# Performance work log

Measured on AMD Instinct MI355X. Metric: run time of the kernel, lower is better.

## Reference

```python
import jax, jax.numpy as jnp
import numpy as np

B = 65536
D = 512            # resnet18 fc.in_features
NUM_CLASSES = 512  # size of batch_centers
LEVELS = [2048, 1024, 512]


def setup_inputs() -> dict:
    key = jax.random.key(0)
    ks = jax.random.split(key, 8)
    x = jax.random.normal(ks[0], (B, D), dtype=jnp.float32)
    labels = jax.random.randint(ks[1], (B,), 0, NUM_CLASSES, dtype=jnp.int64)
    W0 = jax.random.normal(ks[2], (LEVELS[0], D), dtype=jnp.float32) * 0.02
    b0 = jnp.zeros((LEVELS[0],), dtype=jnp.float32)
    W1 = jax.random.normal(ks[3], (LEVELS[1], LEVELS[0]), dtype=jnp.float32) * 0.02
    b1 = jnp.zeros((LEVELS[1],), dtype=jnp.float32)
    W2 = jax.random.normal(ks[4], (LEVELS[2], LEVELS[1]), dtype=jnp.float32) * 0.02
    b2 = jnp.zeros((LEVELS[2],), dtype=jnp.float32)
    lambda_values = jnp.array([1e-3, 1.0, 1.0, 1.0], dtype=jnp.float32)
    return {"x": x, "W0": W0, "b0": b0, "W1": W1, "b1": b1,
            "W2": W2, "b2": b2, "lambda_values": lambda_values,
            "labels": labels}


def _cross_entropy(logits, labels):
    # mean over batch of -log p(label) (torch CrossEntropyLoss default)
    logp = jax.nn.log_softmax(logits, axis=-1)
    nll = -jnp.take_along_axis(logp, labels[:, None], axis=-1)[:, 0]
    return jnp.mean(nll)


def reference(x, W0, b0, W1, b1, W2, b2, lambda_values, labels):
    # --- per-class scatter-mean centers (vectorized segment reduce) ---
    sums = jax.ops.segment_sum(x, labels, num_segments=NUM_CLASSES)
    counts = jax.ops.segment_sum(jnp.ones((x.shape[0],), x.dtype), labels,
                                 num_segments=NUM_CLASSES)
    centers = jnp.where(counts[:, None] > 0,
                        sums / jnp.maximum(counts, 1.0)[:, None],
                        0.0)  # classes absent from batch keep zero centers
    # --- gather-diff center loss: sum_i ||x_i - c_{y_i}||^2 ---
    diff = x - centers[labels]
    center_loss = jnp.sum(diff * diff)
    # --- cascaded classification heads, CE at each level ---
    h = x
    losses = []
    for W, b in ((W0, b0), (W1, b1), (W2, b2)):
        h = h @ W.T + b
        losses.append(_cross_entropy(h, labels))
    classification_losses = jnp.stack(losses)
    return lambda_values[0] * center_loss + jnp.dot(lambda_values[1:],
                                                    classification_losses)
```

## Files before the change

### kernel.cpp

```cpp
#include <hip/hip_runtime.h>
#include <cstdint>
#include <cstddef>

using f32x4  = __attribute__((ext_vector_type(4))) float;
using i32x4v = __attribute__((ext_vector_type(4))) int;
using i32x8v = __attribute__((ext_vector_type(8))) int;

__device__ __forceinline__ unsigned char f2fp8(float f) {
  return (unsigned char)(__builtin_amdgcn_cvt_pk_fp8_f32(f, f, 0, false) & 0xff);
}

__device__ __forceinline__ float fp8b0(unsigned int w) {
  return __builtin_amdgcn_cvt_f32_fp8(w, 0);
}
__device__ __forceinline__ float fp8b1(unsigned int w) {
  return __builtin_amdgcn_cvt_f32_fp8(w, 1);
}
__device__ __forceinline__ float fp8b2(unsigned int w) {
  return __builtin_amdgcn_cvt_f32_fp8(w, 2);
}
__device__ __forceinline__ float fp8b3(unsigned int w) {
  return __builtin_amdgcn_cvt_f32_fp8(w, 3);
}

__device__ __forceinline__ float waveRed(float v) {
#pragma unroll
  for (int m = 32; m >= 1; m >>= 1) v += __shfl_xor(v, m, 64);
  return v;
}

__device__ __forceinline__ void gload16(const void* g, void* l) {
  __builtin_amdgcn_global_load_lds(
      (__attribute__((address_space(1))) uint32_t*)(uintptr_t)g,
      (__attribute__((address_space(3))) uint32_t*)(uint32_t*)l,
      16, 0, 0);
}

__global__ __launch_bounds__(256) void prep_w(
    const float4* __restrict__ W1, const float4* __restrict__ W2,
    const float4* __restrict__ W0f4, const float* __restrict__ W0,
    const float* __restrict__ b0,
    uint32_t* __restrict__ W1_8, uint32_t* __restrict__ W2_8,
    uint32_t* __restrict__ W0_8, unsigned char* __restrict__ W0t8,
    float* __restrict__ zr, int zwords, float* __restrict__ biascat) {
  __shared__ unsigned char t8[64][65];
  const int b = blockIdx.x;
  const int tid = threadIdx.x;
  if (b < 1024) {
    for (int i = b * 256 + tid; i < 524288; i += 1024 * 256) {
      float4 v = W1[i];
      int p = __builtin_amdgcn_cvt_pk_fp8_f32(v.x, v.y, 0, false);
      p = __builtin_amdgcn_cvt_pk_fp8_f32(v.z, v.w, p, true);
      W1_8[i] = (uint32_t)p;
    }
  } else if (b < 1280) {
    for (int i = (b - 1024) * 256 + tid; i < 131072; i += 256 * 256) {
      float4 v = W2[i];
      int p = __builtin_amdgcn_cvt_pk_fp8_f32(v.x, v.y, 0, false);
      p = __builtin_amdgcn_cvt_pk_fp8_f32(v.z, v.w, p, true);
      W2_8[i] = (uint32_t)p;
    }
  } else if (b < 1536) {
    for (int i = (b - 1280) * 256 + tid; i < 262144; i += 256 * 256) {
      float4 v = W0f4[i];
      int p = __builtin_amdgcn_cvt_pk_fp8_f32(v.x, v.y, 0, false);
      p = __builtin_amdgcn_cvt_pk_fp8_f32(v.z, v.w, p, true);
      W0_8[i] = (uint32_t)p;
    }
  } else if (b < 1792) {
    const int t = b - 1536;
    const int r0 = (t >> 3) * 64, c0 = (t & 7) * 64;
#pragma unroll
    for (int p = 0; p < 16; ++p) {
      const int row = p * 4 + (tid >> 6), col = tid & 63;
      t8[row][col] = f2fp8(W0[(size_t)(r0 + row) * 512 + c0 + col]);
    }
    __syncthreads();
#pragma unroll
    for (int p = 0; p < 16; ++p) {
      const int oc = p * 4 + (tid >> 6), orr = tid & 63;
      W0t8[(size_t)(c0 + oc) * 2048 + r0 + orr] = t8[orr][oc];
    }
  } else {
    const int zb = (zwords + 255) >> 8;
    if (b < 1792 + zb) {
      const int i = (b - 1792) * 256 + tid;
      if (i < zwords) zr[i] = 0.f;
    } else {
      const int i = (b - 1792 - zb) * 256 + tid;
      if (i < 2048) biascat[i] = b0[i];
    }
  }
}

__global__ __launch_bounds__(256) void count_k(const int* __restrict__ lab,
                                               int* __restrict__ counts, int n) {
  __shared__ int h[512];
  for (int i = threadIdx.x; i < 512; i += 256) h[i] = 0;
  __syncthreads();
  for (int i = blockIdx.x * 256 + threadIdx.x; i < n; i += gridDim.x * 256)
    atomicAdd(&h[lab[i]], 1);
  __syncthreads();
  for (int i = threadIdx.x; i < 512; i += 256) {
    int v = h[i];
    if (v) atomicAdd(&counts[i], v);
  }
}

__global__ void prefix_k(const int* __restrict__ counts, int* __restrict__ offsets,
                         int* __restrict__ cursor, int nc) {
  const int lane = threadIdx.x;
  int base = 0;
  for (int c0 = 0; c0 < nc; c0 += 64) {
    int v = counts[c0 + lane];
    int x = v;
#pragma unroll
    for (int d = 1; d < 64; d <<= 1) {
      int y = __shfl_up(x, d, 64);
      if (lane >= d) x += y;
    }
    int excl = base + x - v;
    offsets[c0 + lane] = excl;
    cursor[c0 + lane] = excl;
    base += __shfl(x, 63, 64);
  }
}

__global__ void scatter_k(const int* __restrict__ lab, int* __restrict__ cursor,
                          int* __restrict__ buckets, int n) {
  for (int i = blockIdx.x * 256 + threadIdx.x; i < n; i += gridDim.x * 256) {
    int pos = atomicAdd(&cursor[lab[i]], 1);
    buckets[pos] = i;
  }
}

__global__ __launch_bounds__(256) void csum_k(const float* __restrict__ x,
    const int* __restrict__ buckets, const int* __restrict__ offsets,
    const int* __restrict__ counts, float* __restrict__ centers4,
    float* __restrict__ scal) {
  const int c = blockIdx.x >> 2, q = blockIdx.x & 3;
  const int cnt = counts[c];
  const int t = threadIdx.x;
  float sx = 0.f, sy = 0.f, ssq = 0.f;
  if (cnt) {
    const int beg = offsets[c];
    const int lo = beg + (cnt * q) / 4, hi = beg + (cnt * (q + 1)) / 4;
    for (int i = lo; i < hi; ++i) {
      const int row = buckets[i];
      const float2 v = ((const float2*)(x + (size_t)row * 512))[t];
      sx += v.x;
      sy += v.y;
      ssq += v.x * v.x + v.y * v.y;
    }
  }
  float2* dst = (float2*)(centers4 + (size_t)((c << 2) + q) * 512);
  dst[t] = make_float2(sx, sy);
  ssq = waveRed(ssq);
  __shared__ float red[4];
  if ((t & 63) == 0) red[t >> 6] = ssq;
  __syncthreads();
  if (t == 0) {
    const float s = red[0] + red[1] + red[2] + red[3];
    if (s != 0.f) atomicAdd(&scal[0], s);
  }
}

__global__ __launch_bounds__(256) void cnorm_k(const float* __restrict__ centers4,
    float* __restrict__ centers, const int* __restrict__ counts,
    float* __restrict__ out) {
  const int c = blockIdx.x;
  const int t = threadIdx.x;
  const float2* p = (const float2*)(centers4 + (size_t)(c << 2) * 512);
  float2 s = p[t];
  float2 s1 = p[t + 256], s2 = p[t + 512], s3 = p[t + 768];
  s.x += s1.x + s2.x + s3.x;
  s.y += s1.y + s2.y + s3.y;
  ((float2*)(centers + (size_t)c * 512))[t] = s;
  const int cnt = counts[c];
  if (cnt == 0) return;
  float ssq = s.x * s.x + s.y * s.y;
  ssq = waveRed(ssq);
  __shared__ float red[4];
  if ((t & 63) == 0) red[t >> 6] = ssq;
  __syncthreads();
  if (t == 0)
    atomicAdd(out, (red[0] + red[1] + red[2] + red[3]) / (float)cnt);
}

__global__ __launch_bounds__(256) void matvec_k(const float* __restrict__ W,
    const float* __restrict__ vin, const float* __restrict__ badd,
    float* __restrict__ vout, int K) {
  int row = blockIdx.x;
  float s = 0.f;
  for (int k = threadIdx.x; k < K; k += 256) s += W[(size_t)row * K + k] * vin[k];
  s = waveRed(s);
  __shared__ float red[4];
  if ((threadIdx.x & 63) == 0) red[threadIdx.x >> 6] = s;
  __syncthreads();
  if (threadIdx.x == 0) vout[row] = red[0] + red[1] + red[2] + red[3] + badd[row];
}

__global__ void pk_k(const float* __restrict__ centers,
                     const unsigned char* __restrict__ Bcat8,
                     const float* __restrict__ biascat,
                     const int* __restrict__ counts, float* __restrict__ scal) {
  const int b = blockIdx.x;
  const int lvl = b >> 9;
  const int c = b & 511;
  const int lane = threadIdx.x;
  const int cbase = (lvl == 0) ? 0 : (lvl == 1) ? 2048 : 3072;
  const float4* S = (const float4*)(centers + (size_t)c * 512);
  const uint2 wb = ((const uint2*)(Bcat8 + (size_t)(cbase + c) * 512))[lane];
  const float4 s0 = S[lane * 2];
  const float4 s1 = S[lane * 2 + 1];
  float s = s0.x * fp8b0(wb.x) + s0.y * fp8b1(wb.x) +
            s0.z * fp8b2(wb.x) + s0.w * fp8b3(wb.x) +
            s1.x * fp8b0(wb.y) + s1.y * fp8b1(wb.y) +
            s1.z * fp8b2(wb.y) + s1.w * fp8b3(wb.y);
  s = waveRed(s);
  if (lane == 0)
    atomicAdd(&scal[5 + lvl], s + (float)counts[c] * biascat[cbase + c]);
}

__global__ __launch_bounds__(256) void gemm8_w(
    const unsigned char* __restrict__ A8, const unsigned char* __restrict__ B8,
    int M, int N, int K, unsigned char* __restrict__ C8,
    unsigned char* __restrict__ Ct8) {
  __shared__ __align__(16) unsigned char As[128 * 128];
  __shared__ __align__(16) unsigned char Bs[128 * 128];
  const int tid = threadIdx.x;
  const int lane = tid & 63;
  const int wave = tid >> 6;
  const int lane16 = lane & 15;
  const int quad = lane >> 4;
  const int wm = (wave >> 1) * 64;
  const int wn = (wave & 1) * 64;
  const int m0 = blockIdx.y * 128;
  const int n0 = blockIdx.x * 128;

  f32x4 acc[4][4] = {};

  int srow[4], goff[4];
#pragma unroll
  for (int q = 0; q < 4; ++q) {
    const int s = tid + q * 256;
    const int row = s >> 3;
    const int c16 = s & 7;
    srow[q] = row;
    goff[q] = (((c16 >> 1) ^ (row & 3)) << 5) + ((c16 & 1) << 4);
  }

  for (int kt = 0; kt < K; kt += 128) {
#pragma unroll
    for (int q = 0; q < 4; ++q) {
      const int s = tid + q * 256;
      gload16(A8 + (size_t)(m0 + srow[q]) * K + kt + goff[q], &As[s * 16]);
      gload16(B8 + (size_t)(n0 + srow[q]) * K + kt + goff[q], &Bs[s * 16]);
    }
    __syncthreads();
    i32x8v a8[4], b8[4];
#pragma unroll
    for (int i = 0; i < 4; ++i) {
      const int row = i * 16 + lane16;
      const int sc = quad ^ (row & 3);
      const unsigned char* pa = &As[row * 128 + sc * 32];
      const i32x4v lo = *(const i32x4v*)pa;
      const i32x4v hi = *(const i32x4v*)(pa + 16);
      a8[i] = (i32x8v){lo[0], lo[1], lo[2], lo[3], hi[0], hi[1], hi[2], hi[3]};
    }
#pragma unroll
    for (int j = 0; j < 4; ++j) {
      const int row = j * 16 + lane16;
      const int sc = quad ^ (row & 3);
      const unsigned char* pb = &Bs[row * 128 + sc * 32];
      const i32x4v lo = *(const i32x4v*)pb;
      const i32x4v hi = *(const i32x4v*)(pb + 16);
      b8[j] = (i32x8v){lo[0], lo[1], lo[2], lo[3], hi[0], hi[1], hi[2], hi[3]};
    }
#pragma unroll
    for (int i = 0; i < 4; ++i)
#pragma unroll
      for (int j = 0; j < 4; ++j)
        acc[i][j] = __builtin_amdgcn_mfma_scale_f32_16x16x128_f8f6f4(
            a8[i], b8[j], acc[i][j], 0, 0, 0, 0x7f7f7f7f, 0, 0x7f7f7f7f);
    __syncthreads();
  }
#pragma unroll
  for (int i = 0; i < 4; ++i)
#pragma unroll
    for (int r = 0; r < 4; ++r) {
      const int rowg = m0 + wm + i * 16 + quad * 4 + r;
#pragma unroll
      for (int j = 0; j < 4; ++j) {
        const int colg = n0 + wn + j * 16 + lane16;
        const unsigned char v8 = f2fp8(acc[i][j][r]);
        C8[(size_t)rowg * N + colg] = v8;
        if (Ct8) Ct8[(size_t)colg * M + rowg] = v8;
      }
    }
}

__global__ void reorder_k(const unsigned char* __restrict__ in,
                          unsigned char* __restrict__ out) {
  const int id = blockIdx.x * 256 + threadIdx.x;
  const int col = id >> 4;
  const int k32 = id & 15;
  const int kt = k32 >> 2, quad = k32 & 3;
  const int l = quad * 16 + (col & 15);
  const size_t src = (size_t)col * 512 + k32 * 32;
  const size_t fragbase = (size_t)(col >> 6) * 32768 + (size_t)kt * 8192 +
                          (size_t)((col >> 4) & 3) * 2048;
  const uint4 a = *(const uint4*)(in + src);
  const uint4 b = *(const uint4*)(in + src + 16);
  *(uint4*)(out + fragbase + l * 16) = a;
  *(uint4*)(out + fragbase + 1024 + l * 16) = b;
}

__global__ __launch_bounds__(256, 2) void gemm_ce8(
    const float* __restrict__ x, const unsigned char* __restrict__ Bp,
    const float* __restrict__ bias, float* __restrict__ scal) {
  __shared__ __align__(16) unsigned char Bl[4][8192];
  __shared__ float biasl[3584];
  const int tid = threadIdx.x;
  const int lane = tid & 63;
  const int wave = tid >> 6;
  const int lane16 = lane & 15;
  const int quad = lane >> 4;
  const int m0 = blockIdx.x * 128 + wave * 32;

  for (int i = tid; i < 3584; i += 256) biasl[i] = bias[i];

  i32x8v a[2][4];
#pragma unroll
  for (int i = 0; i < 2; ++i) {
    const float* xr = x + (size_t)(m0 + i * 16 + lane16) * 512 + quad * 32;
#pragma unroll
    for (int kt = 0; kt < 4; ++kt) {
      const float4* p4 = (const float4*)(xr + kt * 128);
      int d[8];
#pragma unroll
      for (int p = 0; p < 8; ++p) {
        const float4 f = p4[p];
        int w_ = __builtin_amdgcn_cvt_pk_fp8_f32(f.x, f.y, 0, false);
        w_ = __builtin_amdgcn_cvt_pk_fp8_f32(f.z, f.w, w_, true);
        d[p] = w_;
      }
      a[i][kt] = (i32x8v){d[0], d[1], d[2], d[3], d[4], d[5], d[6], d[7]};
    }
  }
  __syncthreads();

  const int soff = wave * 2048 + lane * 16;
  gload16(Bp + soff, &Bl[0][soff]);
  gload16(Bp + soff + 1024, &Bl[0][soff + 1024]);
  const unsigned char* bsrc = Bp + soff + 8192;

  float es[8];
#pragma unroll
  for (int k = 0; k < 8; ++k) es[k] = 0.f;

  int tile = 0;
#pragma unroll 1
  for (int lvl = 0; lvl < 3; ++lvl) {
    const int nt = (lvl == 0) ? 32 : (lvl == 1) ? 16 : 8;
#pragma unroll 1
    for (int t = 0; t < nt; ++t, ++tile) {
      f32x4 acc[2][4] = {};
#pragma unroll
      for (int ks = 0; ks < 4; ++ks) {
        const int nslot = (ks + 1) & 3;
        gload16(bsrc, &Bl[nslot][soff]);
        gload16(bsrc + 1024, &Bl[nslot][soff + 1024]);
        bsrc += 8192;
        asm volatile("s_waitcnt vmcnt(2)" ::: "memory");
        asm volatile("s_barrier" ::: "memory");
        const unsigned char* bb = &Bl[ks][0];
        i32x8v b8[4];
#pragma unroll
        for (int j = 0; j < 4; ++j) {
          const i32x4v lo = *(const i32x4v*)(bb + j * 2048 + lane * 16);
          const i32x4v hi = *(const i32x4v*)(bb + j * 2048 + 1024 + lane * 16);
          b8[j] = (i32x8v){lo[0], lo[1], lo[2], lo[3],
                           hi[0], hi[1], hi[2], hi[3]};
        }
#pragma unroll
        for (int i = 0; i < 2; ++i)
#pragma unroll
          for (int j = 0; j < 4; ++j)
            acc[i][j] = __builtin_amdgcn_mfma_scale_f32_16x16x128_f8f6f4(
                a[i][ks], b8[j], acc[i][j], 0, 0, 0, 0x7f7f7f7f, 0,
                0x7f7f7f7f);
      }
      float bj[4];
#pragma unroll
      for (int j = 0; j < 4; ++j) bj[j] = biasl[tile * 64 + j * 16 + lane16];
#pragma unroll
      for (int i = 0; i < 2; ++i)
#pragma unroll
        for (int r = 0; r < 4; ++r) {
          float e = 0.f;
#pragma unroll
          for (int j = 0; j < 4; ++j) e += __expf(acc[i][j][r] + bj[j]);
          es[i * 4 + r] += e;
        }
    }
    float ls = 0.f;
#pragma unroll
    for (int k = 0; k < 8; ++k) {
      float tot = es[k];
      tot += __shfl_xor(tot, 1, 64);
      tot += __shfl_xor(tot, 2, 64);
      tot += __shfl_xor(tot, 4, 64);
      tot += __shfl_xor(tot, 8, 64);
      if (lane16 == 0) ls += __logf(tot);
      es[k] = 0.f;
    }
    ls = waveRed(ls);
    if (lane == 0) atomicAdd(&scal[2 + lvl], ls);
  }
}

__global__ void fin_k(const float* __restrict__ scal, const float* __restrict__ lam,
                      float* __restrict__ out, float invB) {
  if (threadIdx.x == 0 && blockIdx.x == 0)
    out[0] = lam[0] * (scal[0] - scal[1]) +
             (lam[1] * (scal[2] - scal[5]) + lam[2] * (scal[3] - scal[6]) +
              lam[3] * (scal[4] - scal[7])) * invB;
}

extern "C" void kernel_launch(void* const* d_in, const int* in_sizes, int n_in,
                              void* d_out, int out_size, void* d_ws, size_t ws_size,
                              hipStream_t stream) {
  const float* x   = (const float*)d_in[0];
  const float* W0  = (const float*)d_in[1];
  const float* b0  = (const float*)d_in[2];
  const float* W1  = (const float*)d_in[3];
  const float* b1  = (const float*)d_in[4];
  const float* W2  = (const float*)d_in[5];
  const float* b2  = (const float*)d_in[6];
  const float* lam = (const float*)d_in[7];
  const int*   lab = (const int*)d_in[8];

  const int Bsz = in_sizes[8];
  const int D   = in_sizes[0] / Bsz;
  const int N0  = in_sizes[2];
  const int N1  = in_sizes[4];
  const int N2  = in_sizes[6];
  const int Ncat = N0 + N1 + N2;
  const int NCLS = 512;

  char* w = (char*)d_ws;
  size_t off = 0;
  auto alloc = [&](size_t bytes) -> void* {
    void* p = w + off;
    off += (bytes + 255) & ~(size_t)255;
    return p;
  };

  unsigned char* Bcat8 = (unsigned char*)alloc((size_t)Ncat * D);
  unsigned char* Bp    = (unsigned char*)alloc((size_t)Ncat * D + 16384);
  unsigned char* W1_8  = (unsigned char*)alloc((size_t)N1 * N0);
  unsigned char* W2_8  = (unsigned char*)alloc((size_t)N2 * N1);
  unsigned char* W0t8  = (unsigned char*)alloc((size_t)D * N0);
  unsigned char* M1t8  = (unsigned char*)alloc((size_t)D * N1);
  float* biascat  = (float*)alloc((size_t)Ncat * 4);
  int* offsets = (int*)alloc(NCLS * 4);
  int* cursor  = (int*)alloc(NCLS * 4);
  int* buckets = (int*)alloc((size_t)Bsz * 4);
  float* centers4 = (float*)alloc((size_t)NCLS * 512 * 4 * 4);
  float* centers  = (float*)alloc((size_t)NCLS * 512 * 4);
  const int zwords = NCLS + 8;
  char* zr = (char*)alloc((size_t)zwords * 4);
  int*   counts  = (int*)zr;
  float* scal    = (float*)(zr + NCLS * 4);
  (void)ws_size; (void)n_in; (void)out_size;

  const int zb = (zwords + 255) / 256;
  prep_w<<<dim3(1792 + zb + 8), dim3(256), 0, stream>>>(
      (const float4*)W1, (const float4*)W2, (const float4*)W0, W0, b0,
      (uint32_t*)W1_8, (uint32_t*)W2_8, (uint32_t*)Bcat8, W0t8,
      (float*)zr, zwords, biascat);

  count_k<<<dim3(32), dim3(256), 0, stream>>>(lab, counts, Bsz);
  prefix_k<<<dim3(1), dim3(64), 0, stream>>>(counts, offsets, cursor, NCLS);
  scatter_k<<<dim3(256), dim3(256), 0, stream>>>(lab, cursor, buckets, Bsz);
  csum_k<<<dim3(4 * NCLS), dim3(256), 0, stream>>>(x, buckets, offsets, counts,
                                                   centers4, scal);
  cnorm_k<<<dim3(NCLS), dim3(256), 0, stream>>>(centers4, centers, counts,
                                                &scal[1]);

  matvec_k<<<dim3(N1), dim3(256), 0, stream>>>(W1, b0, b1, biascat + N0, N0);
  matvec_k<<<dim3(N2), dim3(256), 0, stream>>>(W2, biascat + N0, b2, biascat + N0 + N1, N1);

  gemm8_w<<<dim3(D / 128, N1 / 128), dim3(256), 0, stream>>>(
      W1_8, W0t8, N1, D, N0, Bcat8 + (size_t)N0 * D, M1t8);
  gemm8_w<<<dim3(D / 128, N2 / 128), dim3(256), 0, stream>>>(
      W2_8, M1t8, N2, D, N1, Bcat8 + (size_t)(N0 + N1) * D, nullptr);

  reorder_k<<<dim3(Ncat * D / 32 / 256), dim3(256), 0, stream>>>(Bcat8, Bp);

  pk_k<<<dim3(3 * NCLS), dim3(64), 0, stream>>>(centers, Bcat8, biascat,
                                                counts, scal);

  gemm_ce8<<<dim3(Bsz / 128), dim3(256), 0, stream>>>(x, Bp, biascat, scal);

  fin_k<<<dim3(1), dim3(64), 0, stream>>>(scal, lam, (float*)d_out, 1.f / (float)Bsz);
}
```

Baseline: 517.2 us.

## Deepen B-tile prefetch to three stages and double-buffer LDS reads into registers

Measured after the change: 523.1 us. No clear change (+1.1%).

```diff
diff --git a/kernel.cpp b/kernel.cpp
--- a/kernel.cpp
+++ b/kernel.cpp
@@ -351,13 +351,62 @@
   __syncthreads();
 
   const int soff = wave * 2048 + lane * 16;
-  gload16(Bp + soff, &Bl[0][soff]);
-  gload16(Bp + soff + 1024, &Bl[0][soff + 1024]);
-  const unsigned char* bsrc = Bp + soff + 8192;
+  const unsigned char* bsrc = Bp + soff;
+#pragma unroll
+  for (int c = 0; c < 3; ++c) {
+    gload16(bsrc, &Bl[c][soff]);
+    gload16(bsrc + 1024, &Bl[c][soff + 1024]);
+    bsrc += 8192;
+  }
+  int sc = 3;
+  asm volatile("s_waitcnt vmcnt(4)" ::: "memory");
+  __builtin_amdgcn_s_barrier();
+
+  i32x8v bX[4], bY[4];
+  {
+    const unsigned char* bb = &Bl[0][0];
+#pragma unroll
+    for (int j = 0; j < 4; ++j) {
+      const i32x4v lo = *(const i32x4v*)(bb + j * 2048 + lane * 16);
+      const i32x4v hi = *(const i32x4v*)(bb + j * 2048 + 1024 + lane * 16);
+      bX[j] = (i32x8v){lo[0], lo[1], lo[2], lo[3], hi[0], hi[1], hi[2], hi[3]};
+    }
+  }
 
   float es[8];
 #pragma unroll
   for (int k = 0; k < 8; ++k) es[k] = 0.f;
+
+#define KSTEP(KS, BCUR, BNXT)                                                 \
+  {                                                                           \
+    gload16(bsrc, &Bl[(KS + 3) & 3][soff]);                                   \
+    gload16(bsrc + 1024, &Bl[(KS + 3) & 3][soff + 1024]);                     \
+    bsrc += 8192;                                                             \
+    if (++sc == 224) { sc = 0; bsrc = Bp + soff; }                            \
+    asm volatile("s_waitcnt vmcnt(4)" ::: "memory");                          \
+    __builtin_amdgcn_s_barrier();                                             \
+    {                                                                         \
+      const unsigned char* bb = &Bl[(KS + 1) & 3][0];                         \
+      _Pragma("unroll")                                                       \
+      for (int j = 0; j < 4; ++j) {                                           \
+        const i32x4v lo = *(const i32x4v*)(bb + j * 2048 + lane * 16);        \
+        const i32x4v hi = *(const i32x4v*)(bb + j * 2048 + 1024 + lane * 16); \
+        BNXT[j] = (i32x8v){lo[0], lo[1], lo[2], lo[3],                        \
+                           hi[0], hi[1], hi[2], hi[3]};                       \
+      }                                                                       \
+    }                                                                         \
+    asm volatile("s_waitcnt lgkmcnt(8)" ::: "memory");                        \
+    __builtin_amdgcn_sched_barrier(0);                                        \
+    __builtin_amdgcn_s_setprio(1);                                            \
+    _Pragma("unroll")                                                         \
+    for (int i = 0; i < 2; ++i)                                               \
+      _Pragma("unroll")                                                       \
+      for (int j = 0; j < 4; ++j)                                             \
+        acc[i][j] = __builtin_amdgcn_mfma_scale_f32_16x16x128_f8f6f4(         \
+            a[i][KS], BCUR[j], acc[i][j], 0, 0, 0, 0x7f7f7f7f, 0,             \
+            0x7f7f7f7f);                                                      \
+    __builtin_amdgcn_s_setprio(0);                                            \
+  }
 
   int tile = 0;
 #pragma unroll 1
@@ -366,31 +415,10 @@
 #pragma unroll 1
     for (int t = 0; t < nt; ++t, ++tile) {
       f32x4 acc[2][4] = {};
-#pragma unroll
-      for (int ks = 0; ks < 4; ++ks) {
-        const int nslot = (ks + 1) & 3;
-        gload16(bsrc, &Bl[nslot][soff]);
-        gload16(bsrc + 1024, &Bl[nslot][soff + 1024]);
-        bsrc += 8192;
-        asm volatile("s_waitcnt vmcnt(2)" ::: "memory");
-        asm volatile("s_barrier" ::: "memory");
-        const unsigned char* bb = &Bl[ks][0];
-        i32x8v b8[4];
-#pragma unroll
-        for (int j = 0; j < 4; ++j) {
-          const i32x4v lo = *(const i32x4v*)(bb + j * 2048 + lane * 16);
-          const i32x4v hi = *(const i32x4v*)(bb + j * 2048 + 1024 + lane * 16);
-          b8[j] = (i32x8v){lo[0], lo[1], lo[2], lo[3],
-                           hi[0], hi[1], hi[2], hi[3]};
-        }
-#pragma unroll
-        for (int i = 0; i < 2; ++i)
-#pragma unroll
-          for (int j = 0; j < 4; ++j)
-            acc[i][j] = __builtin_amdgcn_mfma_scale_f32_16x16x128_f8f6f4(
-                a[i][ks], b8[j], acc[i][j], 0, 0, 0, 0x7f7f7f7f, 0,
-                0x7f7f7f7f);
-      }
+      KSTEP(0, bX, bY)
+      KSTEP(1, bY, bX)
+      KSTEP(2, bX, bY)
+      KSTEP(3, bY, bX)
       float bj[4];
 #pragma unroll
       for (int j = 0; j < 4; ++j) bj[j] = biasl[tile * 64 + j * 16 + lane16];
@@ -418,6 +446,7 @@
     ls = waveRed(ls);
     if (lane == 0) atomicAdd(&scal[2 + lvl], ls);
   }
+#undef KSTEP
 }
 
 __global__ void fin_k(const float* __restrict__ scal, const float* __restrict__ lam,
```
